# Kernel tuning notes

Hardware: AMD Instinct MI355X
Metric: run time of the kernel (lower is better)

## Reference

```python
import jax, jax.numpy as jnp
import numpy as np

NUM_HEADS = 16

def setup_inputs() -> dict:
    key = jax.random.key(0)
    ks = jax.random.split(key, 8)
    L, S, N, E = 2048, 2048, 2, 1024
    return {
        "query": jax.random.normal(ks[0], (L, N, E), jnp.float32),
        "key": jax.random.normal(ks[1], (S, N, E), jnp.float32),
        "value": jax.random.normal(ks[2], (S, N, E), jnp.float32),
        "in_proj_weight": jax.random.normal(ks[3], (3 * E, E), jnp.float32) * (E ** -0.5),
        "in_proj_bias": jax.random.normal(ks[4], (3 * E,), jnp.float32) * 0.01,
        "out_proj_weight": jax.random.normal(ks[5], (E, E), jnp.float32) * (E ** -0.5),
        "out_proj_bias": jax.random.normal(ks[6], (E,), jnp.float32) * 0.01,
        "rel_bias": jax.random.normal(ks[7], (NUM_HEADS, 2 * S - 1), jnp.float32) * 0.02,
    }


def reference(query, key, value, in_proj_weight, in_proj_bias,
              out_proj_weight, out_proj_bias, rel_bias):
    L, N, E = query.shape
    S = key.shape[0]
    H = NUM_HEADS
    D = E // H
    scaling = D ** -0.5

    # in-projection: F.linear(x, W, b) = x @ W.T + b, with W split into q/k/v rows
    wq, wk, wv = jnp.split(in_proj_weight, 3, axis=0)
    bq, bk, bv = jnp.split(in_proj_bias, 3, axis=0)
    q = (query @ wq.T + bq) * scaling          # [L,N,E]
    k = key @ wk.T + bk                        # [S,N,E]
    v = value @ wv.T + bv                      # [S,N,E]

    q = q.reshape(L, N, H, D)
    k = k.reshape(S, N, H, D)
    v = v.reshape(S, N, H, D)

    # attention scores [N,H,L,S]
    scores = jnp.einsum("lnhd,snhd->nhls", q, k)

    # relative-position bias: bias[h,i,j] = rel_bias[h, (i - j) + S - 1]
    rel_idx = jnp.arange(L)[:, None] - jnp.arange(S)[None, :] + (S - 1)  # [L,S]
    bias = rel_bias[:, rel_idx]                # [H,L,S]
    scores = scores + bias[None, :, :, :]

    attn = jax.nn.softmax(scores, axis=-1)     # [N,H,L,S]

    out = jnp.einsum("nhls,snhd->lnhd", attn, v).reshape(L, N, E)
    out = out @ out_proj_weight.T + out_proj_bias  # [L,N,E]
    return out
```

## Files before the change

kernel.cpp:

```cpp
#include <hip/hip_runtime.h>
#include <hip/hip_bf16.h>


typedef __attribute__((ext_vector_type(8))) short bf16x8;
typedef __attribute__((ext_vector_type(4))) float f32x4;

#define LOG2E 1.4426950408889634f

__device__ __forceinline__ unsigned short f2bf(float x) {
  unsigned u = __float_as_uint(x);
  u += 0x7fffu + ((u >> 16) & 1u);
  return (unsigned short)(u >> 16);
}

__device__ __forceinline__ void gld_lds16(const void* g, void* l) {
  __builtin_amdgcn_global_load_lds(
      (const __attribute__((address_space(1))) unsigned int*)g,
      (__attribute__((address_space(3))) unsigned int*)l,
      16, 0, 0);
}

__global__ __launch_bounds__(256) void cvt_bf16(const float* __restrict__ src,
                                                unsigned short* __restrict__ dst,
                                                int n4, float scale) {
  int i = blockIdx.x * 256 + threadIdx.x;
  if (i >= n4) return;
  float4 v = reinterpret_cast<const float4*>(src)[i];
  ushort4 o;
  o.x = f2bf(v.x * scale);
  o.y = f2bf(v.y * scale);
  o.z = f2bf(v.z * scale);
  o.w = f2bf(v.w * scale);
  reinterpret_cast<ushort4*>(dst)[i] = o;
}

template<int OUT_F32, int QKV>
__global__ __launch_bounds__(256) void gemm_nt(const unsigned short* __restrict__ Abase,
                                               const unsigned short* __restrict__ Wbase,
                                               const float* __restrict__ biasBase,
                                               void* __restrict__ outBase) {
  const int K = 1024, Nout = 1024;
  __shared__ __attribute__((aligned(16))) unsigned short As[2][128 * 32];
  __shared__ __attribute__((aligned(16))) unsigned short Bs[2][128 * 32];

  const int tid = threadIdx.x;
  const int l = tid & 63, w = tid >> 6;
  const int lane15 = tid & 15, lhi = (tid >> 4) & 3;
  const int Mbase = blockIdx.y * 128, Nbase = blockIdx.x * 128;
  const int rb = (w >> 1) * 64, cb = (w & 1) * 64;

  const unsigned short* A = Abase;
  const unsigned short* W = Wbase;
  const float* bias = biasBase;
  float biasScale = 1.0f;
  unsigned short* outU = (unsigned short*)outBase;
  float* outF = (float*)outBase;
  if (QKV) {
    const int z = blockIdx.z;
    A    += (size_t)z * 4194304;
    W    += (size_t)z * 1048576;
    bias += z * 1024;
    outU += (size_t)z * 4194304;
    if (z == 0) biasScale = 0.125f * LOG2E;
  }

  auto stage = [&](int kt, int buf) {
#pragma unroll
    for (int i = 0; i < 2; ++i) {
      int u = (i * 4 + w) * 64 + l;
      int row = u >> 2, slot = u & 3;
      int ks = slot ^ ((row >> 1) & 3);
      gld_lds16(A + (size_t)(Mbase + row) * K + kt * 32 + ks * 8,
                &As[buf][(i * 4 + w) * 512]);
      gld_lds16(W + (size_t)(Nbase + row) * K + kt * 32 + ks * 8,
                &Bs[buf][(i * 4 + w) * 512]);
    }
  };

  f32x4 acc[4][4] = {};
  stage(0, 0);
  const int NK = 32;
  for (int kt = 0; kt < NK; ++kt) {
    __syncthreads();
    if (kt + 1 < NK) stage(kt + 1, (kt + 1) & 1);
    const int buf = kt & 1;
    bf16x8 a[4], b[4];
#pragma unroll
    for (int m = 0; m < 4; ++m) {
      int row = rb + m * 16 + lane15;
      a[m] = *(const bf16x8*)&As[buf][row * 32 + (lhi ^ ((row >> 1) & 3)) * 8];
      int col = cb + m * 16 + lane15;
      b[m] = *(const bf16x8*)&Bs[buf][col * 32 + (lhi ^ ((col >> 1) & 3)) * 8];
    }
#pragma unroll
    for (int m = 0; m < 4; ++m)
#pragma unroll
      for (int nt = 0; nt < 4; ++nt)
        acc[m][nt] = __builtin_amdgcn_mfma_f32_16x16x32_bf16(a[m], b[nt], acc[m][nt], 0, 0, 0);
  }

  float bv[4];
#pragma unroll
  for (int nt = 0; nt < 4; ++nt)
    bv[nt] = bias[Nbase + cb + nt * 16 + lane15] * biasScale;
#pragma unroll
  for (int m = 0; m < 4; ++m)
#pragma unroll
    for (int nt = 0; nt < 4; ++nt)
#pragma unroll
      for (int r = 0; r < 4; ++r) {
        float v = acc[m][nt][r] + bv[nt];
        size_t idx = (size_t)(Mbase + rb + m * 16 + lhi * 4 + r) * Nout +
                     (Nbase + cb + nt * 16 + lane15);
        if (OUT_F32) outF[idx] = v;
        else         outU[idx] = f2bf(v);
      }
}

__global__ __launch_bounds__(256) void vtrans(const unsigned short* __restrict__ vP,
                                              unsigned short* __restrict__ vT) {
  __shared__ unsigned short t_lds[64][66];
  const int tid = threadIdx.x;
  const int st = blockIdx.x, nh = blockIdx.y;
  const int n = nh >> 4, h = nh & 15;
  const int sb = st * 64;
#pragma unroll
  for (int r = 0; r < 2; ++r) {
    int idx = tid + r * 256;
    int row = idx >> 3, ch = idx & 7;
    bf16x8 v = *(const bf16x8*)(vP + (size_t)((sb + row) * 2 + n) * 1024 + h * 64 + ch * 8);
#pragma unroll
    for (int j = 0; j < 8; ++j) t_lds[row][ch * 8 + j] = (unsigned short)v[j];
  }
  __syncthreads();
#pragma unroll
  for (int r = 0; r < 2; ++r) {
    int idx = tid + r * 256;
    int d = idx >> 3, sc = idx & 7;
    bf16x8 o;
#pragma unroll
    for (int j = 0; j < 8; ++j) o[j] = (short)t_lds[sc * 8 + j][d];
    *(bf16x8*)(vT + (size_t)(nh * 64 + d) * 2048 + sb + sc * 8) = o;
  }
}

__global__ __launch_bounds__(256) void attn(const unsigned short* __restrict__ qP,
                                            const unsigned short* __restrict__ kP,
                                            const unsigned short* __restrict__ vT,
                                            const float* __restrict__ rel_bias,
                                            unsigned short* __restrict__ attnout) {
  __shared__ float bias_lds[2112];
  __shared__ __attribute__((aligned(16))) unsigned short Ks[64 * 64];
  __shared__ __attribute__((aligned(16))) unsigned short Vs[64 * 64];
  __shared__ __attribute__((aligned(16))) unsigned short Ps[4][16 * 72];

  const int tid = threadIdx.x;
  const int l = tid & 63, w = tid >> 6;
  const int lane15 = tid & 15, lhi = (tid >> 4) & 3;
  const int qt = blockIdx.x, nh = blockIdx.y;
  const int n = nh >> 4, h = nh & 15;
  const int qb = qt * 64;

  for (int j = tid; j < 2111; j += 256) bias_lds[j] = rel_bias[h * 4095 + qb + j] * LOG2E;

  bf16x8 qf[2];
  {
    const unsigned short* qrow = qP + (size_t)((qb + w * 16 + lane15) * 2 + n) * 1024 + h * 64;
    qf[0] = *(const bf16x8*)(qrow + lhi * 8);
    qf[1] = *(const bf16x8*)(qrow + 32 + lhi * 8);
  }

  f32x4 o[4] = {};
  float lsum[4] = {0.f, 0.f, 0.f, 0.f};

  for (int kt = 0; kt < 32; ++kt) {
    __syncthreads();
#pragma unroll
    for (int i = 0; i < 2; ++i) {
      int u = (i * 4 + w) * 64 + l;
      int row = u >> 3, slot = u & 7;
      int ks = slot ^ (row & 7);
      gld_lds16(kP + (size_t)((kt * 64 + row) * 2 + n) * 1024 + h * 64 + ks * 8,
                Ks + (i * 4 + w) * 512);
      gld_lds16(vT + (size_t)(nh * 64 + row) * 2048 + kt * 64 + ks * 8,
                Vs + (i * 4 + w) * 512);
    }
    __syncthreads();

    f32x4 c[4];
#pragma unroll
    for (int sg = 0; sg < 4; ++sg) {
      int srow = sg * 16 + lane15;
      bf16x8 kf0 = *(const bf16x8*)&Ks[srow * 64 + ((0 + lhi) ^ (srow & 7)) * 8];
      bf16x8 kf1 = *(const bf16x8*)&Ks[srow * 64 + ((4 + lhi) ^ (srow & 7)) * 8];
      f32x4 z = {};
      z = __builtin_amdgcn_mfma_f32_16x16x32_bf16(qf[0], kf0, z, 0, 0, 0);
      z = __builtin_amdgcn_mfma_f32_16x16x32_bf16(qf[1], kf1, z, 0, 0, 0);
      c[sg] = z;
    }
#pragma unroll
    for (int sg = 0; sg < 4; ++sg) {
      int s = kt * 64 + sg * 16 + lane15;
#pragma unroll
      for (int r = 0; r < 4; ++r) {
        int lloc = w * 16 + lhi * 4 + r;
        float p = exp2f(c[sg][r] + bias_lds[lloc + 2047 - s]);
        c[sg][r] = p;
        lsum[r] += p;
      }
    }

    unsigned short* pw = &Ps[w][0];
#pragma unroll
    for (int sg = 0; sg < 4; ++sg) {
      int col = sg * 16 + lane15;
      unsigned u01, u23;
      asm("v_cvt_pk_bf16_f32 %0, %1, %2" : "=v"(u01) : "v"(c[sg][0]), "v"(c[sg][1]));
      asm("v_cvt_pk_bf16_f32 %0, %1, %2" : "=v"(u23) : "v"(c[sg][2]), "v"(c[sg][3]));
      pw[(lhi * 4 + 0) * 72 + col] = (unsigned short)u01;
      pw[(lhi * 4 + 1) * 72 + col] = (unsigned short)(u01 >> 16);
      pw[(lhi * 4 + 2) * 72 + col] = (unsigned short)u23;
      pw[(lhi * 4 + 3) * 72 + col] = (unsigned short)(u23 >> 16);
    }
    asm volatile("s_waitcnt lgkmcnt(0)" ::: "memory");

#pragma unroll
    for (int sc = 0; sc < 2; ++sc) {
      bf16x8 pf = *(const bf16x8*)&pw[lane15 * 72 + sc * 32 + lhi * 8];
#pragma unroll
      for (int dg = 0; dg < 4; ++dg) {
        int drow = dg * 16 + lane15;
        bf16x8 vf = *(const bf16x8*)&Vs[drow * 64 + ((sc * 4 + lhi) ^ (drow & 7)) * 8];
        o[dg] = __builtin_amdgcn_mfma_f32_16x16x32_bf16(pf, vf, o[dg], 0, 0, 0);
      }
    }
  }

#pragma unroll
  for (int r = 0; r < 4; ++r) {
    float v = lsum[r];
    v += __shfl_xor(v, 1);
    v += __shfl_xor(v, 2);
    v += __shfl_xor(v, 4);
    v += __shfl_xor(v, 8);
    lsum[r] = 1.0f / v;
  }
#pragma unroll
  for (int dg = 0; dg < 4; ++dg)
#pragma unroll
    for (int r = 0; r < 4; ++r) {
      int ql = qb + w * 16 + lhi * 4 + r;
      int e = h * 64 + dg * 16 + lane15;
      attnout[(size_t)(ql * 2 + n) * 1024 + e] = f2bf(o[dg][r] * lsum[r]);
    }
}

extern "C" void kernel_launch(void* const* d_in, const int* in_sizes, int n_in,
                              void* d_out, int out_size, void* d_ws, size_t ws_size,
                              hipStream_t stream) {
  (void)in_sizes; (void)n_in; (void)out_size; (void)ws_size;
  const float* query = (const float*)d_in[0];
  const float* key   = (const float*)d_in[1];
  const float* value = (const float*)d_in[2];
  const float* w_in  = (const float*)d_in[3];
  const float* b_in  = (const float*)d_in[4];
  const float* w_out = (const float*)d_in[5];
  const float* b_out = (const float*)d_in[6];
  const float* rel_b = (const float*)d_in[7];

  unsigned short* ws   = (unsigned short*)d_ws;
  unsigned short* qA   = ws;
  unsigned short* kA   = ws + 4194304;
  unsigned short* vA   = ws + 8388608;
  unsigned short* wIn  = ws + 12582912;
  unsigned short* wOut = ws + 15728640;
  unsigned short* qP   = ws + 16777216;
  unsigned short* vT   = ws + 29360128;
  unsigned short* attnout = qA;

  cvt_bf16<<<4096, 256, 0, stream>>>(query, qA, 1048576, 1.0f);
  cvt_bf16<<<4096, 256, 0, stream>>>(key,   kA, 1048576, 1.0f);
  cvt_bf16<<<4096, 256, 0, stream>>>(value, vA, 1048576, 1.0f);
  cvt_bf16<<<1024, 256, 0, stream>>>(w_in,            wIn,            262144, 0.125f * LOG2E);
  cvt_bf16<<<2048, 256, 0, stream>>>(w_in + 1048576,  wIn + 1048576,  524288, 1.0f);
  cvt_bf16<<<1024, 256, 0, stream>>>(w_out, wOut, 262144, 1.0f);

  dim3 gQKV(8, 32, 3);
  gemm_nt<0, 1><<<gQKV, 256, 0, stream>>>(qA, wIn, b_in, qP);

  dim3 g32(32, 32);
  vtrans<<<g32, 256, 0, stream>>>(qP + 2 * 4194304, vT);
  attn<<<g32, 256, 0, stream>>>(qP, qP + 4194304, vT, rel_b, attnout);

  dim3 gOUT(8, 32, 1);
  gemm_nt<1, 0><<<gOUT, 256, 0, stream>>>(attnout, wOut, b_out, d_out);
}
```

Baseline: 276.2 us.

## Rewrite attention with 32x32 MFMA, double-buffered K/V, register P, fused converts

The attention kernel now handles 128 queries per block with 32x32x16 MFMAs and computes S^T so the probabilities stay in registers; permlane32 swaps replace the LDS round-trip for P. K/V tiles are double-buffered so the next tile loads while the current one is computed. Bias is preloaded as the MFMA accumulator from four shifted copies, and the row sum comes from an extra MFMA against ones. The six conversion launches are merged into two. In exchange, the grid has half as many blocks, the kernel uses more LDS and registers, and it does an extra matrix op per tile.

```diff
diff --git a/kernel.cpp b/kernel.cpp
--- a/kernel.cpp
+++ b/kernel.cpp
@@ -4,6 +4,8 @@
 
 typedef __attribute__((ext_vector_type(8))) short bf16x8;
 typedef __attribute__((ext_vector_type(4))) float f32x4;
+typedef __attribute__((ext_vector_type(16))) float f32x16;
+typedef __attribute__((ext_vector_type(4))) unsigned int u32x4;
 
 #define LOG2E 1.4426950408889634f
 
@@ -20,18 +22,38 @@
       16, 0, 0);
 }
 
-__global__ __launch_bounds__(256) void cvt_bf16(const float* __restrict__ src,
-                                                unsigned short* __restrict__ dst,
-                                                int n4, float scale) {
+__global__ __launch_bounds__(256) void cvt_qkv(const float* __restrict__ q,
+                                               const float* __restrict__ k,
+                                               const float* __restrict__ v,
+                                               unsigned short* __restrict__ dst) {
+  const int z = blockIdx.y;
+  const float* src = (z == 0) ? q : (z == 1) ? k : v;
   int i = blockIdx.x * 256 + threadIdx.x;
-  if (i >= n4) return;
-  float4 v = reinterpret_cast<const float4*>(src)[i];
+  float4 vv = reinterpret_cast<const float4*>(src)[i];
   ushort4 o;
-  o.x = f2bf(v.x * scale);
-  o.y = f2bf(v.y * scale);
-  o.z = f2bf(v.z * scale);
-  o.w = f2bf(v.w * scale);
-  reinterpret_cast<ushort4*>(dst)[i] = o;
+  o.x = f2bf(vv.x); o.y = f2bf(vv.y); o.z = f2bf(vv.z); o.w = f2bf(vv.w);
+  reinterpret_cast<ushort4*>(dst + (size_t)z * 4194304)[i] = o;
+}
+
+__global__ __launch_bounds__(256) void cvt_w(const float* __restrict__ w_in,
+                                             const float* __restrict__ w_out,
+                                             unsigned short* __restrict__ wIn,
+                                             unsigned short* __restrict__ wOut) {
+  int i = blockIdx.x * 256 + threadIdx.x;
+  if (i < 786432) {
+    float scale = (i < 262144) ? 0.125f * LOG2E : 1.0f;
+    float4 vv = reinterpret_cast<const float4*>(w_in)[i];
+    ushort4 o;
+    o.x = f2bf(vv.x * scale); o.y = f2bf(vv.y * scale);
+    o.z = f2bf(vv.z * scale); o.w = f2bf(vv.w * scale);
+    reinterpret_cast<ushort4*>(wIn)[i] = o;
+  } else {
+    int j = i - 786432;
+    float4 vv = reinterpret_cast<const float4*>(w_out)[j];
+    ushort4 o;
+    o.x = f2bf(vv.x); o.y = f2bf(vv.y); o.z = f2bf(vv.z); o.w = f2bf(vv.w);
+    reinterpret_cast<ushort4*>(wOut)[j] = o;
+  }
 }
 
 template<int OUT_F32, int QKV>
@@ -149,110 +171,119 @@
                                             const unsigned short* __restrict__ vT,
                                             const float* __restrict__ rel_bias,
                                             unsigned short* __restrict__ attnout) {
-  __shared__ float bias_lds[2112];
-  __shared__ __attribute__((aligned(16))) unsigned short Ks[64 * 64];
-  __shared__ __attribute__((aligned(16))) unsigned short Vs[64 * 64];
-  __shared__ __attribute__((aligned(16))) unsigned short Ps[4][16 * 72];
+  __shared__ __attribute__((aligned(16))) float bias4[4 * 2180];
+  __shared__ __attribute__((aligned(16))) unsigned short Ks[2][4096];
+  __shared__ __attribute__((aligned(16))) unsigned short Vs[2][4096];
 
   const int tid = threadIdx.x;
   const int l = tid & 63, w = tid >> 6;
-  const int lane15 = tid & 15, lhi = (tid >> 4) & 3;
+  const int l31 = tid & 31, lh5 = (tid >> 5) & 1;
   const int qt = blockIdx.x, nh = blockIdx.y;
   const int n = nh >> 4, h = nh & 15;
-  const int qb = qt * 64;
-
-  for (int j = tid; j < 2111; j += 256) bias_lds[j] = rel_bias[h * 4095 + qb + j] * LOG2E;
-
-  bf16x8 qf[2];
+  const int qb = qt * 128;
+  const int wq = w * 32;
+  const int lloc = wq + l31;
+
+#pragma unroll
+  for (int m = 0; m < 4; ++m)
+    for (int i = tid; i < 2176; i += 256) {
+      int src = qb + i + m;
+      bias4[m * 2180 + i] = (src <= 4094) ? rel_bias[h * 4095 + src] * LOG2E : 0.f;
+    }
+
+  bf16x8 qf[4];
   {
-    const unsigned short* qrow = qP + (size_t)((qb + w * 16 + lane15) * 2 + n) * 1024 + h * 64;
-    qf[0] = *(const bf16x8*)(qrow + lhi * 8);
-    qf[1] = *(const bf16x8*)(qrow + 32 + lhi * 8);
-  }
-
-  f32x4 o[4] = {};
-  float lsum[4] = {0.f, 0.f, 0.f, 0.f};
-
-  for (int kt = 0; kt < 32; ++kt) {
-    __syncthreads();
+    const unsigned short* qrow = qP + (size_t)((qb + lloc) * 2 + n) * 1024 + h * 64;
+#pragma unroll
+    for (int m16 = 0; m16 < 4; ++m16)
+      qf[m16] = *(const bf16x8*)(qrow + m16 * 16 + lh5 * 8);
+  }
+
+  const short one_bf = (short)0x3F80;
+  bf16x8 ones = {one_bf, one_bf, one_bf, one_bf, one_bf, one_bf, one_bf, one_bf};
+
+  f32x16 o0 = {}, o1 = {}, osum = {};
+
+  auto stage = [&](int kt, int buf) {
 #pragma unroll
     for (int i = 0; i < 2; ++i) {
       int u = (i * 4 + w) * 64 + l;
       int row = u >> 3, slot = u & 7;
       int ks = slot ^ (row & 7);
       gld_lds16(kP + (size_t)((kt * 64 + row) * 2 + n) * 1024 + h * 64 + ks * 8,
-                Ks + (i * 4 + w) * 512);
+                &Ks[buf][(i * 4 + w) * 512]);
       gld_lds16(vT + (size_t)(nh * 64 + row) * 2048 + kt * 64 + ks * 8,
-                Vs + (i * 4 + w) * 512);
-    }
+                &Vs[buf][(i * 4 + w) * 512]);
+    }
+  };
+
+  stage(0, 0);
+  for (int kt = 0; kt < 32; ++kt) {
     __syncthreads();
-
-    f32x4 c[4];
-#pragma unroll
-    for (int sg = 0; sg < 4; ++sg) {
-      int srow = sg * 16 + lane15;
-      bf16x8 kf0 = *(const bf16x8*)&Ks[srow * 64 + ((0 + lhi) ^ (srow & 7)) * 8];
-      bf16x8 kf1 = *(const bf16x8*)&Ks[srow * 64 + ((4 + lhi) ^ (srow & 7)) * 8];
-      f32x4 z = {};
-      z = __builtin_amdgcn_mfma_f32_16x16x32_bf16(qf[0], kf0, z, 0, 0, 0);
-      z = __builtin_amdgcn_mfma_f32_16x16x32_bf16(qf[1], kf1, z, 0, 0, 0);
-      c[sg] = z;
-    }
-#pragma unroll
-    for (int sg = 0; sg < 4; ++sg) {
-      int s = kt * 64 + sg * 16 + lane15;
-#pragma unroll
-      for (int r = 0; r < 4; ++r) {
-        int lloc = w * 16 + lhi * 4 + r;
-        float p = exp2f(c[sg][r] + bias_lds[lloc + 2047 - s]);
-        c[sg][r] = p;
-        lsum[r] += p;
+    if (kt + 1 < 32) stage(kt + 1, (kt + 1) & 1);
+    const int buf = kt & 1;
+
+#pragma unroll
+    for (int sb = 0; sb < 2; ++sb) {
+      const int srow = sb * 32 + l31;
+      bf16x8 kf[4];
+#pragma unroll
+      for (int m16 = 0; m16 < 4; ++m16)
+        kf[m16] = *(const bf16x8*)&Ks[buf][srow * 64 + (((m16 * 2 + lh5) ^ (srow & 7)) * 8)];
+
+      f32x16 c;
+#pragma unroll
+      for (int rg = 0; rg < 4; ++rg) {
+        int a = lloc + 2047 - (kt * 64 + sb * 32 + rg * 8 + lh5 * 4) - 3;
+        const float4 f4 = *(const float4*)&bias4[(a & 3) * 2180 + (a & ~3)];
+        c[rg * 4 + 0] = f4.w; c[rg * 4 + 1] = f4.z;
+        c[rg * 4 + 2] = f4.y; c[rg * 4 + 3] = f4.x;
       }
-    }
-
-    unsigned short* pw = &Ps[w][0];
-#pragma unroll
-    for (int sg = 0; sg < 4; ++sg) {
-      int col = sg * 16 + lane15;
-      unsigned u01, u23;
-      asm("v_cvt_pk_bf16_f32 %0, %1, %2" : "=v"(u01) : "v"(c[sg][0]), "v"(c[sg][1]));
-      asm("v_cvt_pk_bf16_f32 %0, %1, %2" : "=v"(u23) : "v"(c[sg][2]), "v"(c[sg][3]));
-      pw[(lhi * 4 + 0) * 72 + col] = (unsigned short)u01;
-      pw[(lhi * 4 + 1) * 72 + col] = (unsigned short)(u01 >> 16);
-      pw[(lhi * 4 + 2) * 72 + col] = (unsigned short)u23;
-      pw[(lhi * 4 + 3) * 72 + col] = (unsigned short)(u23 >> 16);
-    }
-    asm volatile("s_waitcnt lgkmcnt(0)" ::: "memory");
-
-#pragma unroll
-    for (int sc = 0; sc < 2; ++sc) {
-      bf16x8 pf = *(const bf16x8*)&pw[lane15 * 72 + sc * 32 + lhi * 8];
-#pragma unroll
-      for (int dg = 0; dg < 4; ++dg) {
-        int drow = dg * 16 + lane15;
-        bf16x8 vf = *(const bf16x8*)&Vs[drow * 64 + ((sc * 4 + lhi) ^ (drow & 7)) * 8];
-        o[dg] = __builtin_amdgcn_mfma_f32_16x16x32_bf16(pf, vf, o[dg], 0, 0, 0);
+
+#pragma unroll
+      for (int m16 = 0; m16 < 4; ++m16)
+        c = __builtin_amdgcn_mfma_f32_32x32x16_bf16(kf[m16], qf[m16], c, 0, 0, 0);
+
+      float p[16];
+#pragma unroll
+      for (int i = 0; i < 16; ++i) p[i] = exp2f(c[i]);
+
+      unsigned pk0[4], pk1[4];
+#pragma unroll
+      for (int rg = 0; rg < 4; ++rg) {
+        asm("v_cvt_pk_bf16_f32 %0, %1, %2" : "=v"(pk0[rg]) : "v"(p[rg * 4 + 0]), "v"(p[rg * 4 + 1]));
+        asm("v_cvt_pk_bf16_f32 %0, %1, %2" : "=v"(pk1[rg]) : "v"(p[rg * 4 + 2]), "v"(p[rg * 4 + 3]));
       }
-    }
-  }
-
-#pragma unroll
-  for (int r = 0; r < 4; ++r) {
-    float v = lsum[r];
-    v += __shfl_xor(v, 1);
-    v += __shfl_xor(v, 2);
-    v += __shfl_xor(v, 4);
-    v += __shfl_xor(v, 8);
-    lsum[r] = 1.0f / v;
-  }
-#pragma unroll
-  for (int dg = 0; dg < 4; ++dg)
-#pragma unroll
-    for (int r = 0; r < 4; ++r) {
-      int ql = qb + w * 16 + lhi * 4 + r;
-      int e = h * 64 + dg * 16 + lane15;
-      attnout[(size_t)(ql * 2 + n) * 1024 + e] = f2bf(o[dg][r] * lsum[r]);
-    }
+
+#pragma unroll
+      for (int t = 0; t < 2; ++t) {
+        unsigned x0 = pk0[t * 2 + 0], y0 = pk0[t * 2 + 1];
+        unsigned x1 = pk1[t * 2 + 0], y1 = pk1[t * 2 + 1];
+        asm("v_permlane32_swap_b32 %0, %1" : "+v"(x0), "+v"(y0));
+        asm("v_permlane32_swap_b32 %0, %1" : "+v"(x1), "+v"(y1));
+        u32x4 pu; pu[0] = x0; pu[1] = x1; pu[2] = y0; pu[3] = y1;
+        bf16x8 pa = __builtin_bit_cast(bf16x8, pu);
+        const int tb = sb * 2 + t;
+#pragma unroll
+        for (int dn = 0; dn < 2; ++dn) {
+          int drow = dn * 32 + l31;
+          bf16x8 vf = *(const bf16x8*)&Vs[buf][drow * 64 + (((tb * 2 + lh5) ^ (drow & 7)) * 8)];
+          if (dn == 0) o0 = __builtin_amdgcn_mfma_f32_32x32x16_bf16(pa, vf, o0, 0, 0, 0);
+          else         o1 = __builtin_amdgcn_mfma_f32_32x32x16_bf16(pa, vf, o1, 0, 0, 0);
+        }
+        osum = __builtin_amdgcn_mfma_f32_32x32x16_bf16(pa, ones, osum, 0, 0, 0);
+      }
+    }
+  }
+
+#pragma unroll
+  for (int reg = 0; reg < 16; ++reg) {
+    float inv = 1.0f / osum[reg];
+    int lrow = qb + wq + (reg & 3) + 8 * (reg >> 2) + 4 * lh5;
+    size_t base = (size_t)(lrow * 2 + n) * 1024 + h * 64 + l31;
+    attnout[base]      = f2bf(o0[reg] * inv);
+    attnout[base + 32] = f2bf(o1[reg] * inv);
+  }
 }
 
 extern "C" void kernel_launch(void* const* d_in, const int* in_sizes, int n_in,
@@ -269,28 +300,24 @@
   const float* rel_b = (const float*)d_in[7];
 
   unsigned short* ws   = (unsigned short*)d_ws;
-  unsigned short* qA   = ws;
-  unsigned short* kA   = ws + 4194304;
-  unsigned short* vA   = ws + 8388608;
+  unsigned short* qkvA = ws;
   unsigned short* wIn  = ws + 12582912;
   unsigned short* wOut = ws + 15728640;
   unsigned short* qP   = ws + 16777216;
   unsigned short* vT   = ws + 29360128;
-  unsigned short* attnout = qA;
-
-  cvt_bf16<<<4096, 256, 0, stream>>>(query, qA, 1048576, 1.0f);
-  cvt_bf16<<<4096, 256, 0, stream>>>(key,   kA, 1048576, 1.0f);
-  cvt_bf16<<<4096, 256, 0, stream>>>(value, vA, 1048576, 1.0f);
-  cvt_bf16<<<1024, 256, 0, stream>>>(w_in,            wIn,            262144, 0.125f * LOG2E);
-  cvt_bf16<<<2048, 256, 0, stream>>>(w_in + 1048576,  wIn + 1048576,  524288, 1.0f);
-  cvt_bf16<<<1024, 256, 0, stream>>>(w_out, wOut, 262144, 1.0f);
+  unsigned short* attnout = qkvA;
+
+  dim3 gC(4096, 3);
+  cvt_qkv<<<gC, 256, 0, stream>>>(query, key, value, qkvA);
+  cvt_w<<<4096, 256, 0, stream>>>(w_in, w_out, wIn, wOut);
 
   dim3 gQKV(8, 32, 3);
-  gemm_nt<0, 1><<<gQKV, 256, 0, stream>>>(qA, wIn, b_in, qP);
+  gemm_nt<0, 1><<<gQKV, 256, 0, stream>>>(qkvA, wIn, b_in, qP);
 
   dim3 g32(32, 32);
   vtrans<<<g32, 256, 0, stream>>>(qP + 2 * 4194304, vT);
-  attn<<<g32, 256, 0, stream>>>(qP, qP + 4194304, vT, rel_b, attnout);
+  dim3 gA(16, 32);
+  attn<<<gA, 256, 0, stream>>>(qP, qP + 4194304, vT, rel_b, attnout);
 
   dim3 gOUT(8, 32, 1);
   gemm_nt<1, 0><<<gOUT, 256, 0, stream>>>(attnout, wOut, b_out, d_out);
```

Measured after the change: 271.2 us. Within noise of the previous version (-1.8%).
